# Kernel tuning notes

Measured on AMD Instinct MI355X. Metric: run time of the kernel, lower is better.

The kernel has to match this reference:

```python
import jax, jax.numpy as jnp
import numpy as np

S, N, F, E, H = 64, 1000, 64, 128, 2  # seq_len, nodes/graph, node_dim, emb_dim, heads
DEG = 8
C = E // H  # per-head channels


def setup_inputs() -> dict:
    key = jax.random.key(0)
    ks = jax.random.split(key, 16)
    Ntot = S * N
    Eg = N * DEG
    src = jax.random.randint(ks[0], (S, Eg), 0, N)
    dst = jax.random.randint(ks[1], (S, Eg), 0, N)
    off = (jnp.arange(S) * N)[:, None]
    edge_index = jnp.stack([(src + off).reshape(-1), (dst + off).reshape(-1)]).astype(jnp.int32)
    nfm = jax.random.normal(ks[2], (Ntot, F), jnp.float32)
    reachable = jax.random.uniform(ks[3], (S, N)) > 0.2
    reachable = reachable.at[:, 0].set(True)  # ensure each row has a reachable node
    h0 = jnp.zeros((N, E), jnp.float32)
    c0 = jnp.zeros((N, E), jnp.float32)

    def lin(k, i, o):
        return (jax.random.normal(k, (i, o), jnp.float32) / np.sqrt(i)).astype(jnp.float32)

    return dict(
        nfm=nfm, edge_index=edge_index, reachable=reachable, h0=h0, c0=c0,
        gat_W1=lin(ks[4], F, E), gat_b1=jnp.zeros((E,), jnp.float32),
        gat_att1=(jax.random.normal(ks[5], (H, C), jnp.float32) / np.sqrt(C)).astype(jnp.float32),
        gat_bias1=jnp.zeros((E,), jnp.float32),
        gat_W=(jax.random.normal(ks[6], (4, E, E), jnp.float32) / np.sqrt(E)).astype(jnp.float32),
        gat_b=jnp.zeros((4, E), jnp.float32),
        gat_att=(jax.random.normal(ks[7], (4, H, C), jnp.float32) / np.sqrt(C)).astype(jnp.float32),
        gat_bias=jnp.zeros((4, E), jnp.float32),
        lstm_Wih=(jax.random.normal(ks[8], (4 * E, E), jnp.float32) / np.sqrt(E)).astype(jnp.float32),
        lstm_Whh=(jax.random.normal(ks[9], (4 * E, E), jnp.float32) / np.sqrt(E)).astype(jnp.float32),
        lstm_bih=jnp.zeros((4 * E,), jnp.float32), lstm_bhh=jnp.zeros((4 * E,), jnp.float32),
        th6_W=lin(ks[10], E, E), th6_b=jnp.zeros((E,), jnp.float32),
        th7_W=lin(ks[11], E, E), th7_b=jnp.zeros((E,), jnp.float32),
        th5_W=lin(ks[12], 2 * E, 1), th5_b=jnp.zeros((1,), jnp.float32),
    )


def _gat_layer(x, src, dst, W, b, att, bias, Ntot):
    # GATv2Conv, share_weights=True: x_l == x_r = lin(x)
    Hh, Ch = att.shape
    xl = (x @ W + b).reshape(-1, Hh, Ch)                 # [Ntot,H,C]
    e = jax.nn.leaky_relu(xl[src] + xl[dst], 0.2)        # [Etot,H,C]
    logit = jnp.einsum('ehc,hc->eh', e, att)             # [Etot,H]
    m = jax.ops.segment_max(logit, dst, num_segments=Ntot)
    a = jnp.exp(logit - m[dst])                          # segment-stable softmax
    denom = jax.ops.segment_sum(a, dst, num_segments=Ntot)
    alpha = a / denom[dst]
    out = jax.ops.segment_sum(xl[src] * alpha[:, :, None], dst, num_segments=Ntot)
    return out.reshape(-1, Hh * Ch) + bias               # concat heads + bias


def _forward(nfm, edge_index, reachable, h0, c0, gat_W1, gat_b1, gat_att1, gat_bias1,
             gat_W, gat_b, gat_att, gat_bias, lstm_Wih, lstm_Whh, lstm_bih, lstm_bhh,
             th6_W, th6_b, th7_W, th7_b, th5_W, th5_b):
    Ntot = nfm.shape[0]
    loops = jnp.arange(Ntot, dtype=edge_index.dtype)     # add_self_loops=True
    src = jnp.concatenate([edge_index[0], loops])
    dst = jnp.concatenate([edge_index[1], loops])

    x = jax.nn.relu(_gat_layer(nfm, src, dst, gat_W1, gat_b1, gat_att1, gat_bias1, Ntot))
    for i in range(4):  # layers 2..5; no activation after last
        x = _gat_layer(x, src, dst, gat_W[i], gat_b[i], gat_att[i], gat_bias[i], Ntot)
        if i < 3:
            x = jax.nn.relu(x)

    mu = x.reshape(S, N, E)                              # [seq, batch(=nodes), emb]

    def step(carry, xt):
        h, c = carry
        g = xt @ lstm_Wih.T + lstm_bih + h @ lstm_Whh.T + lstm_bhh
        i_, f_, gg, o_ = jnp.split(g, 4, axis=-1)        # torch gate order i,f,g,o
        c = jax.nn.sigmoid(f_) * c + jax.nn.sigmoid(i_) * jnp.tanh(gg)
        h = jax.nn.sigmoid(o_) * jnp.tanh(c)
        return (h, c), h

    (hT, cT), mu = jax.lax.scan(step, (h0, c0), mu)      # mu: [S,N,E]

    meanpool = mu.mean(axis=1, keepdims=True)            # [S,1,E]
    gs = meanpool @ th6_W + th6_b
    la = mu @ th7_W + th7_b
    rep = jax.nn.relu(jnp.concatenate([jnp.broadcast_to(gs, la.shape), la], axis=-1))
    logits = (rep @ th5_W)[..., 0] + th5_b               # [S,N]
    logits = jnp.where(reachable, logits, -jnp.inf)
    prob = jax.nn.softmax(logits, axis=1)
    return prob, hT, cT


def reference(nfm, edge_index, reachable, h0, c0, gat_W1, gat_b1, gat_att1, gat_bias1,
              gat_W, gat_b, gat_att, gat_bias, lstm_Wih, lstm_Whh, lstm_bih, lstm_bhh,
              th6_W, th6_b, th7_W, th7_b, th5_W, th5_b):
    return _forward(nfm, edge_index, reachable, h0, c0, gat_W1, gat_b1, gat_att1, gat_bias1,
                    gat_W, gat_b, gat_att, gat_bias, lstm_Wih, lstm_Whh, lstm_bih, lstm_bhh,
                    th6_W, th6_b, th7_W, th7_b, th5_W, th5_b)
```

## Files before the change

kernel.cpp:

```cpp
#include <hip/hip_runtime.h>
#include <hip/hip_bf16.h>

#define SQ   64
#define NN   1000
#define NT   64000
#define EE   128
#define EG   512000
#define ET   576000

#define WS_XA      0ull
#define WS_XB      33000000ull
#define WS_ROWPTR  66000000ull
#define WS_CURSOR  66300000ull
#define WS_SRCS    66600000ull
#define WS_INCL    69000000ull
#define WS_BSUM    69300000ull
#define WS_BOFF    69302048ull
#define WS_MODE    69304096ull
#define WS_WQA     70000000ull
#define WS_WQB     70262144ull
#define WS_AS      70600000ull
#define WS_LOGIT2  70700000ull
#define WS2_XC     33000000ull
#define WS2_BFRAG  164100000ull
#define WS2_GHI    164300000ull
#define WS2_GLO    164650000ull
#define WS2_B512   165000000ull
#define WS2_MODE   165010000ull
#define WS2_AS     165020000ull
#define WS2_LOGIT2 165100000ull
#define WS2_NEED   165360000ull
#define G_W1    0
#define G_WL    8192
#define G_PROJ  73728
#define G_W7    139264

typedef __attribute__((ext_vector_type(8))) short short8;
typedef __attribute__((ext_vector_type(4))) float f32x4;

__device__ __forceinline__ float rdlane(float v, int l) {
    return __int_as_float(__builtin_amdgcn_readlane(__float_as_int(v), l));
}
__device__ __forceinline__ float sigm(float x) { return 1.0f / (1.0f + __expf(-x)); }
__device__ __forceinline__ float tanh_f(float x) {
    x = fminf(fmaxf(x, -30.0f), 30.0f);
    float e = __expf(2.0f * x);
    return (e - 1.0f) / (e + 1.0f);
}
__device__ __forceinline__ float tanh2(float x) {
    return 2.0f / (1.0f + __expf(-2.0f * x)) - 1.0f;
}
__device__ __forceinline__ ushort f2bf(float x) {
    unsigned u = __float_as_uint(x);
    unsigned r = (u + 0x7FFFu + ((u >> 16) & 1u)) >> 16;
    return (ushort)r;
}
__device__ __forceinline__ float bf2f(ushort h) {
    return __uint_as_float(((unsigned)h) << 16);
}

__global__ void detect_mode_k(const unsigned char* __restrict__ p, int* __restrict__ mode) {
    __shared__ int f0, f3;
    const int t = threadIdx.x;
    if (t == 0) { f0 = 0; f3 = 0; }
    __syncthreads();
    int l0 = 0, l3 = 0;
    for (int i = t; i < 16000; i += 256) {
        if (p[4 * i])     l0 = 1;
        if (p[4 * i + 3]) l3 = 1;
    }
    if (l0) atomicOr(&f0, 1);
    if (l3) atomicOr(&f3, 1);
    __syncthreads();
    if (t == 0) {
        int m;
        if (f0 && f3)      m = 1;
        else if (f0)       m = 0;
        else               m = 2;
        *mode = m;
    }
}

__global__ void zero_ints_k(int* __restrict__ p, int n) {
    int i = blockIdx.x * 256 + threadIdx.x;
    if (i < n) p[i] = 0;
}
__global__ void hist_k(const int* __restrict__ ei, int* __restrict__ deg) {
    int e = blockIdx.x * 256 + threadIdx.x;
    if (e < ET) {
        int d = (e < EG) ? ei[EG + e] : (e - EG);
        atomicAdd(deg + d, 1);
    }
}
__global__ void scan1_k(const int* __restrict__ deg, int* __restrict__ incl, int* __restrict__ bsum) {
    __shared__ int sh[256];
    const int t = threadIdx.x;
    const int i = blockIdx.x * 256 + t;
    sh[t] = deg[i];
    __syncthreads();
    for (int o = 1; o < 256; o <<= 1) {
        int add = (t >= o) ? sh[t - o] : 0;
        __syncthreads();
        sh[t] += add;
        __syncthreads();
    }
    incl[i] = sh[t];
    if (t == 255) bsum[blockIdx.x] = sh[255];
}
__global__ void scan2_k(const int* __restrict__ bsum, int* __restrict__ boff) {
    __shared__ int sh[256];
    const int t = threadIdx.x;
    int v = (t < 250) ? bsum[t] : 0;
    sh[t] = v;
    __syncthreads();
    for (int o = 1; o < 256; o <<= 1) {
        int add = (t >= o) ? sh[t - o] : 0;
        __syncthreads();
        sh[t] += add;
        __syncthreads();
    }
    if (t < 250) boff[t] = sh[t] - v;
}
__global__ void scan3_k(const int* __restrict__ incl, const int* __restrict__ boff,
                        int* __restrict__ rowptr, int* __restrict__ cursor_deg) {
    const int i = blockIdx.x * 256 + threadIdx.x;
    int total = incl[i] + boff[blockIdx.x];
    int excl  = total - cursor_deg[i];
    rowptr[i] = excl;
    cursor_deg[i] = excl;
    if (i == NT - 1) rowptr[NT] = total;
}
__global__ void fill_k(const int* __restrict__ ei, int* __restrict__ cursor, int* __restrict__ srcs) {
    int e = blockIdx.x * 256 + threadIdx.x;
    if (e < ET) {
        int s_, d_;
        if (e < EG) { s_ = ei[e]; d_ = ei[EG + e]; }
        else        { s_ = e - EG; d_ = s_; }
        int p = atomicAdd(cursor + d_, 1);
        srcs[p] = s_;
    }
}

__device__ __forceinline__ void gfrag_dev(const float* __restrict__ src, const int ks,
                                          const int ns, const int K,
                                          ushort* __restrict__ dhi, ushort* __restrict__ dlo,
                                          const int total, const int id) {
    if (id < total) {
        int j = id & 7, lane = (id >> 3) & 63;
        int f = id >> 9;
        int KT = K >> 5;
        int nt = f / KT, kt = f - nt * KT;
        int n = nt * 16 + (lane & 15);
        int k = kt * 32 + ((lane >> 4) << 3) + j;
        float v = src[(size_t)k * ks + (size_t)n * ns];
        ushort h = f2bf(v);
        dhi[id] = h;
        dlo[id] = f2bf(v - bf2f(h));
    }
}
__global__ void build_all_k(const float* __restrict__ Whh, const float* __restrict__ bih,
                            const float* __restrict__ bhh, const float* __restrict__ W1,
                            const float* __restrict__ Wl, const float* __restrict__ Wih,
                            const float* __restrict__ W7, ushort* __restrict__ Bfrag,
                            float* __restrict__ b512, ushort* __restrict__ ghi,
                            ushort* __restrict__ glo) {
    const int b = blockIdx.x, t = threadIdx.x;
    if (b < 256) {
        int id = b * 256 + t;
        int j = id & 7, lane = (id >> 3) & 63, kt = (id >> 9) & 3, tile = id >> 11;
        int gate = tile * 16 + (lane & 15);
        int k = kt * 32 + ((lane >> 4) << 3) + j;
        Bfrag[id] = f2bf(Whh[(size_t)gate * 128 + k]);
    } else if (b < 258) {
        int i = (b - 256) * 256 + t;
        if (i < 512) b512[i] = bih[i] + bhh[i];
    } else if (b < 290) {
        gfrag_dev(W1, 128, 1, 64, ghi + G_W1, glo + G_W1, 8192, (b - 258) * 256 + t);
    } else if (b < 546) {
        int bb = b - 290;
        int i = bb >> 6;
        gfrag_dev(Wl + (size_t)i * 16384, 128, 1, 128,
                  ghi + G_WL + i * 16384, glo + G_WL + i * 16384, 16384, (bb & 63) * 256 + t);
    } else if (b < 802) {
        gfrag_dev(Wih, 1, 128, 128, ghi + G_PROJ, glo + G_PROJ, 65536, (b - 546) * 256 + t);
    } else {
        gfrag_dev(W7, 128, 1, 128, ghi + G_W7, glo + G_W7, 16384, (b - 802) * 256 + t);
    }
}

template <int KT>
__global__ __launch_bounds__(256) void gemm_mf(
    const float* __restrict__ x, const ushort* __restrict__ bhi,
    const ushort* __restrict__ blo, const float* __restrict__ bias,
    float* __restrict__ out, const int ldout)
{
    constexpr int K = KT * 32;
    __shared__ __align__(16) ushort ahi_s[KT * 4 * 64 * 8];
    __shared__ __align__(16) ushort alo_s[KT * 4 * 64 * 8];
    const int t = threadIdx.x;
    const int w = t >> 6, lane = t & 63;
    const int quad = lane >> 4, col = lane & 15;
    const int row0 = blockIdx.x * 64;
    const int col0 = blockIdx.y * 128;

    {
        const int r  = t >> 2;
        const int kc = (t & 3) * (K / 4);
        const int rw = r >> 4, rcol = r & 15;
        const float* xr = x + (size_t)(row0 + r) * K + kc;
#pragma unroll
        for (int k = 0; k < K / 4; k += 4) {
            const int ch = kc + k;
            const int idx = (((ch >> 5) * 4 + rw) * 64 + ((ch >> 3) & 3) * 16 + rcol) * 8
                            + (ch & 7);
            float4 v = *(const float4*)(xr + k);
            ushort h0_ = f2bf(v.x), h1_ = f2bf(v.y), h2_ = f2bf(v.z), h3_ = f2bf(v.w);
            ushort l0_ = f2bf(v.x - bf2f(h0_)), l1_ = f2bf(v.y - bf2f(h1_));
            ushort l2_ = f2bf(v.z - bf2f(h2_)), l3_ = f2bf(v.w - bf2f(h3_));
            *(uint2*)(ahi_s + idx) = make_uint2((uint)h0_ | ((uint)h1_ << 16),
                                                (uint)h2_ | ((uint)h3_ << 16));
            *(uint2*)(alo_s + idx) = make_uint2((uint)l0_ | ((uint)l1_ << 16),
                                                (uint)l2_ | ((uint)l3_ << 16));
        }
    }
    __syncthreads();

    short8 ah[KT], al[KT];
#pragma unroll
    for (int kt = 0; kt < KT; kt++) {
        const int off = ((kt * 4 + w) * 64 + lane) * 8;
        ah[kt] = *(const short8*)(ahi_s + off);
        al[kt] = *(const short8*)(alo_s + off);
    }

    f32x4 acc[8];
#pragma unroll
    for (int q = 0; q < 8; q++) acc[q] = (f32x4){0.f, 0.f, 0.f, 0.f};

#pragma unroll
    for (int q = 0; q < 8; q++) {
#pragma unroll
        for (int kt = 0; kt < KT; kt++) {
            const int f = ((((col0 >> 4) + q) * KT + kt) * 64 + lane) * 8;
            short8 bh = *(const short8*)(bhi + f);
            short8 bl = *(const short8*)(blo + f);
            acc[q] = __builtin_amdgcn_mfma_f32_16x16x32_bf16(ah[kt], bh, acc[q], 0, 0, 0);
            acc[q] = __builtin_amdgcn_mfma_f32_16x16x32_bf16(al[kt], bh, acc[q], 0, 0, 0);
            acc[q] = __builtin_amdgcn_mfma_f32_16x16x32_bf16(ah[kt], bl, acc[q], 0, 0, 0);
        }
    }

#pragma unroll
    for (int q = 0; q < 8; q++) {
        float bv = bias[col0 + q * 16 + col];
#pragma unroll
        for (int r = 0; r < 4; r++) {
            out[(size_t)(row0 + w * 16 + quad * 4 + r) * ldout + col0 + q * 16 + col]
                = acc[q][r] + bv;
        }
    }
}

template <int K>
__global__ __launch_bounds__(256) void gemm3(
    const float* __restrict__ x, const float* __restrict__ W,
    const float* __restrict__ b, float* __restrict__ out)
{
    __shared__ float Wsh[64 * 128];
    __shared__ float xT[64][132];
    const int t = threadIdx.x;
    const int row0 = blockIdx.x * 128;
    const int cg = t & 15;
    const int rg = t >> 4;
    float4 acc[8][2];
#pragma unroll
    for (int r = 0; r < 8; r++) {
        acc[r][0] = make_float4(0.f, 0.f, 0.f, 0.f);
        acc[r][1] = make_float4(0.f, 0.f, 0.f, 0.f);
    }
    for (int k0 = 0; k0 < K; k0 += 64) {
        for (int i = t * 4; i < 64 * 128; i += 1024)
            *(float4*)(Wsh + i) = *(const float4*)(W + (size_t)k0 * 128 + i);
        for (int i = t * 4; i < 128 * 64; i += 1024) {
            int r = i >> 6, k = i & 63;
            float4 v = *(const float4*)(x + (size_t)(row0 + r) * K + k0 + k);
            xT[k + 0][r] = v.x; xT[k + 1][r] = v.y;
            xT[k + 2][r] = v.z; xT[k + 3][r] = v.w;
        }
        __syncthreads();
#pragma unroll 2
        for (int k = 0; k < 64; k++) {
            float4 w0 = *(const float4*)(Wsh + k * 128 + cg * 8);
            float4 w1 = *(const float4*)(Wsh + k * 128 + cg * 8 + 4);
            float4 x0 = *(const float4*)(&xT[k][rg * 8]);
            float4 x1 = *(const float4*)(&xT[k][rg * 8 + 4]);
            float xv[8] = {x0.x, x0.y, x0.z, x0.w, x1.x, x1.y, x1.z, x1.w};
#pragma unroll
            for (int r = 0; r < 8; r++) {
                acc[r][0].x += xv[r] * w0.x; acc[r][0].y += xv[r] * w0.y;
                acc[r][0].z += xv[r] * w0.z; acc[r][0].w += xv[r] * w0.w;
                acc[r][1].x += xv[r] * w1.x; acc[r][1].y += xv[r] * w1.y;
                acc[r][1].z += xv[r] * w1.z; acc[r][1].w += xv[r] * w1.w;
            }
        }
        __syncthreads();
    }
    float4 bv0 = *(const float4*)(b + cg * 8);
    float4 bv1 = *(const float4*)(b + cg * 8 + 4);
#pragma unroll
    for (int r = 0; r < 8; r++) {
        float4 o0, o1;
        o0.x = acc[r][0].x + bv0.x; o0.y = acc[r][0].y + bv0.y;
        o0.z = acc[r][0].z + bv0.z; o0.w = acc[r][0].w + bv0.w;
        o1.x = acc[r][1].x + bv1.x; o1.y = acc[r][1].y + bv1.y;
        o1.z = acc[r][1].z + bv1.z; o1.w = acc[r][1].w + bv1.w;
        float* op = out + (size_t)(row0 + rg * 8 + r) * 128 + cg * 8;
        *(float4*)(op) = o0;
        *(float4*)(op + 4) = o1;
    }
}

__global__ __launch_bounds__(256) void gat_fused_k(
    const float* __restrict__ xl, const int* __restrict__ rowptr,
    const int* __restrict__ srcs, const float* __restrict__ att,
    const float* __restrict__ bias, float* __restrict__ out, const int do_relu)
{
    const int lane = threadIdx.x & 63;
    const int q = lane & 31;
    const int h = lane >> 5;
    const int b = blockIdx.x;
    const int g = b & 7;
    const int j = b >> 3;
    const int jq = j / 250;
    const int jj = j - jq * 250;
    const int s = g + 8 * jq;
    const int n = s * NN + jj * 4 + (threadIdx.x >> 6);

    const float4 a4 = *(const float4*)(att + q * 4);
    const float4 xd = *(const float4*)(xl + (size_t)n * 128 + q * 4);
    const int i0 = rowptr[n], i1 = rowptr[n + 1];

    float mA = -1e30f, dA = 0.f, axA = 0.f, ayA = 0.f, azA = 0.f, awA = 0.f;
    float mB = -1e30f, dB = 0.f, axB = 0.f, ayB = 0.f, azB = 0.f, awB = 0.f;

    int iA = i0 + h, iB = i0 + h + 2;
    int svA = (iA < i1) ? srcs[iA] : 0;
    int svB = (iB < i1) ? srcs[iB] : 0;
    float4 xsA = *(const float4*)(xl + (size_t)svA * 128 + q * 4);
    float4 xsB = *(const float4*)(xl + (size_t)svB * 128 + q * 4);

    for (int base = i0; base < i1; base += 4) {
        const bool vA = (iA < i1), vB = (iB < i1);
        const int svA2 = (iA + 4 < i1) ? srcs[iA + 4] : 0;
        const int svB2 = (iB + 4 < i1) ? srcs[iB + 4] : 0;
        const float4 xA2 = *(const float4*)(xl + (size_t)svA2 * 128 + q * 4);
        const float4 xB2 = *(const float4*)(xl + (size_t)svB2 * 128 + q * 4);

        float uA0 = xsA.x + xd.x, uA1 = xsA.y + xd.y;
        float uA2 = xsA.z + xd.z, uA3 = xsA.w + xd.w;
        float uB0 = xsB.x + xd.x, uB1 = xsB.y + xd.y;
        float uB2 = xsB.z + xd.z, uB3 = xsB.w + xd.w;
        float pA, pB;
        pA  = a4.x * fmaxf(uA0, 0.2f * uA0);
        pA += a4.y * fmaxf(uA1, 0.2f * uA1);
        pA += a4.z * fmaxf(uA2, 0.2f * uA2);
        pA += a4.w * fmaxf(uA3, 0.2f * uA3);
        pB  = a4.x * fmaxf(uB0, 0.2f * uB0);
        pB += a4.y * fmaxf(uB1, 0.2f * uB1);
        pB += a4.z * fmaxf(uB2, 0.2f * uB2);
        pB += a4.w * fmaxf(uB3, 0.2f * uB3);
        pA += __shfl_xor(pA, 1);   pB += __shfl_xor(pB, 1);
        pA += __shfl_xor(pA, 2);   pB += __shfl_xor(pB, 2);
        pA += __shfl_xor(pA, 4);   pB += __shfl_xor(pB, 4);
        pA += __shfl_xor(pA, 8);   pB += __shfl_xor(pB, 8);

        float mnA = fmaxf(mA, vA ? pA : -1e30f);
        float mnB = fmaxf(mB, vB ? pB : -1e30f);
        float scA = __expf(mA - mnA), scB = __expf(mB - mnB);
        float wA = vA ? __expf(pA - mnA) : 0.f;
        float wB = vB ? __expf(pB - mnB) : 0.f;
        dA  = dA  * scA + wA;          dB  = dB  * scB + wB;
        axA = axA * scA + wA * xsA.x;  axB = axB * scB + wB * xsB.x;
        ayA = ayA * scA + wA * xsA.y;  ayB = ayB * scB + wB * xsB.y;
        azA = azA * scA + wA * xsA.z;  azB = azB * scB + wB * xsB.z;
        awA = awA * scA + wA * xsA.w;  awB = awB * scB + wB * xsB.w;
        mA = mnA; mB = mnB;
        xsA = xA2; xsB = xB2;
        iA += 4; iB += 4;
    }

    float m1 = fmaxf(mA, mB);
    float sA = __expf(mA - m1), sB = __expf(mB - m1);
    float d  = dA * sA + dB * sB;
    float ax = axA * sA + axB * sB;
    float ay = ayA * sA + ayB * sB;
    float az = azA * sA + azB * sB;
    float aw = awA * sA + awB * sB;
    float m  = m1;

    float m2 = __shfl_xor(m, 32);
    float d2 = __shfl_xor(d, 32);
    float bx = __shfl_xor(ax, 32);
    float by = __shfl_xor(ay, 32);
    float bz = __shfl_xor(az, 32);
    float bw = __shfl_xor(aw, 32);
    float mm = fmaxf(m, m2);
    float s1 = __expf(m - mm), s2 = __expf(m2 - mm);
    float den = d * s1 + d2 * s2;
    float inv = 1.f / den;
    float4 bv = *(const float4*)(bias + q * 4);
    float ox = (ax * s1 + bx * s2) * inv + bv.x;
    float oy = (ay * s1 + by * s2) * inv + bv.y;
    float oz = (az * s1 + bz * s2) * inv + bv.z;
    float ow = (aw * s1 + bw * s2) * inv + bv.w;
    if (do_relu) {
        ox = fmaxf(ox, 0.f); oy = fmaxf(oy, 0.f);
        oz = fmaxf(oz, 0.f); ow = fmaxf(ow, 0.f);
    }
    if (lane < 32)
        *(float4*)(out + (size_t)n * 128 + q * 4) = make_float4(ox, oy, oz, ow);
}

__global__ void build_wq_k(const float* __restrict__ Wih, const float* __restrict__ Whh,
                           float4* __restrict__ WQa, float4* __restrict__ WQb) {
    int id = blockIdx.x * 256 + threadIdx.x;
    if (id < 64 * 256) {
        int kp = id >> 8, t = id & 255;
        int j1 = t, j2 = t + 256;
        WQa[id] = make_float4(Wih[(size_t)j1 * 128 + 2 * kp], Whh[(size_t)j1 * 128 + 2 * kp],
                              Wih[(size_t)j1 * 128 + 2 * kp + 1], Whh[(size_t)j1 * 128 + 2 * kp + 1]);
        WQb[id] = make_float4(Wih[(size_t)j2 * 128 + 2 * kp], Whh[(size_t)j2 * 128 + 2 * kp],
                              Wih[(size_t)j2 * 128 + 2 * kp + 1], Whh[(size_t)j2 * 128 + 2 * kp + 1]);
    }
}

#define LSTM_GROUP(buf, gbase)                                                     \
    _Pragma("unroll")                                                              \
    for (int i_ = 0; i_ < 4; i_++) {                                               \
        const int kp_ = (gbase) * 4 + i_;                                          \
        const float4 qa_ = buf[i_];                                                \
        const float4 qb_ = buf[4 + i_];                                            \
        _Pragma("unroll")                                                          \
        for (int n_ = 0; n_ < 4; n_++) {                                           \
            const float sx0_ = rdlane(xr[n_].x, kp_);                              \
            const float sh0_ = rdlane(hr[n_].x, kp_);                              \
            const float sx1_ = rdlane(xr[n_].y, kp_);                              \
            const float sh1_ = rdlane(hr[n_].y, kp_);                              \
            acc1[n_] += sx0_ * qa_.x + sh0_ * qa_.y + sx1_ * qa_.z + sh1_ * qa_.w; \
            acc2[n_] += sx0_ * qb_.x + sh0_ * qb_.y + sx1_ * qb_.z + sh1_ * qb_.w; \
        }                                                                          \
    }

__global__ __launch_bounds__(256, 1) void lstm_k(
    float* __restrict__ mu, const float4* __restrict__ WQa, const float4* __restrict__ WQb,
    const float* __restrict__ bih, const float* __restrict__ bhh,
    const float* __restrict__ h0, const float* __restrict__ c0,
    float* __restrict__ hT, float* __restrict__ cT)
{
    const int t = threadIdx.x, lane = t & 63;
    const int n0 = blockIdx.x * 4;
    __shared__ float hsh[4][128];
    __shared__ float gsh[4][512];
    const float b1 = bih[t] + bhh[t];
    const float b2 = bih[t + 256] + bhh[t + 256];
    float creg[2];
#pragma unroll
    for (int q = 0; q < 2; q++) {
        int id = t + 256 * q;
        creg[q] = c0[(size_t)(n0 + (id >> 7)) * 128 + (id & 127)];
    }
    for (int i = t; i < 512; i += 256)
        hsh[i >> 7][i & 127] = h0[(size_t)(n0 + (i >> 7)) * 128 + (i & 127)];

    const float4* pA = WQa + t;
    const float4* pB = WQb + t;

    float2 xr[4], xnx[4];
#pragma unroll
    for (int n = 0; n < 4; n++)
        xr[n] = *(const float2*)(mu + (size_t)n0 * 128 + n * 128 + lane * 2);
    __syncthreads();

    for (int s = 0; s < SQ; s++) {
        float* xrow = mu + ((size_t)s * NN + n0) * 128;
        float2 hr[4];
#pragma unroll
        for (int n = 0; n < 4; n++) hr[n] = *(const float2*)(&hsh[n][lane * 2]);

        float4 bufA[8], bufB[8];
#pragma unroll
        for (int i = 0; i < 4; i++) { bufA[i] = pA[i * 256]; bufA[4 + i] = pB[i * 256]; }

        if (s + 1 < SQ) {
            const float* xrow2 = mu + ((size_t)(s + 1) * NN + n0) * 128;
#pragma unroll
            for (int n = 0; n < 4; n++) xnx[n] = *(const float2*)(xrow2 + n * 128 + lane * 2);
        }

        float acc1[4], acc2[4];
#pragma unroll
        for (int n = 0; n < 4; n++) { acc1[n] = b1; acc2[n] = b2; }

        for (int g = 0; g < 16; g += 2) {
#pragma unroll
            for (int i = 0; i < 4; i++) {
                bufB[i]     = pA[((g + 1) * 4 + i) * 256];
                bufB[4 + i] = pB[((g + 1) * 4 + i) * 256];
            }
            LSTM_GROUP(bufA, g)
            if (g < 14) {
#pragma unroll
                for (int i = 0; i < 4; i++) {
                    bufA[i]     = pA[((g + 2) * 4 + i) * 256];
                    bufA[4 + i] = pB[((g + 2) * 4 + i) * 256];
                }
            }
            LSTM_GROUP(bufB, g + 1)
        }

#pragma unroll
        for (int n = 0; n < 4; n++) { gsh[n][t] = acc1[n]; gsh[n][t + 256] = acc2[n]; }
        __syncthreads();
#pragma unroll
        for (int q = 0; q < 2; q++) {
            int id = t + 256 * q;
            int n = id >> 7, e = id & 127;
            float iv = gsh[n][e], fv = gsh[n][128 + e];
            float gv = gsh[n][256 + e], ov = gsh[n][384 + e];
            float c = sigm(fv) * creg[q] + sigm(iv) * tanh_f(gv);
            float h = sigm(ov) * tanh_f(c);
            creg[q] = c;
            hsh[n][e] = h;
            xrow[n * 128 + e] = h;
            if (s == SQ - 1) {
                hT[(size_t)(n0 + n) * 128 + e] = h;
                cT[(size_t)(n0 + n) * 128 + e] = c;
            }
        }
#pragma unroll
        for (int n = 0; n < 4; n++) xr[n] = xnx[n];
        __syncthreads();
    }
}

__global__ __launch_bounds__(512, 2) void lstm8_k(
    float* __restrict__ mu, const float* __restrict__ xC,
    const ushort* __restrict__ Bfrag,
    const float* __restrict__ h0, const float* __restrict__ c0,
    float* __restrict__ hT, float* __restrict__ cT)
{
    const int t = threadIdx.x;
    const int w = t >> 6, lane = t & 63;
    const int quad = lane >> 4, col = lane & 15;
    const int n0 = blockIdx.x * 4;
    const int enode = t >> 7;
    const int ech   = t & 127;

    __shared__ __align__(16) ushort hbuf[2][2][16 * 136];
    __shared__ float gsh[4][512];

    short8 bf[4][4];
#pragma unroll
    for (int g4 = 0; g4 < 4; g4++)
#pragma unroll
        for (int kt = 0; kt < 4; kt++) {
            int tile = g4 * 8 + w;
            bf[g4][kt] = *(const short8*)(Bfrag + (((tile * 4 + kt) * 64 + lane) << 3));
        }

    for (int i = t; i < 2048; i += 512) {
        int node = i >> 7, ee = i & 127;
        float v = (node < 4) ? h0[(size_t)(n0 + node) * 128 + ee] : 0.f;
        ushort hh = f2bf(v), hl = f2bf(v - bf2f(hh));
        hbuf[0][0][node * 136 + ee] = hh; hbuf[0][1][node * 136 + ee] = hl;
        hbuf[1][0][node * 136 + ee] = hh; hbuf[1][1][node * 136 + ee] = hl;
    }
    float cst = c0[(size_t)(n0 + enode) * 128 + ech];

    float xcr[4], xcn[4];
#pragma unroll
    for (int g4 = 0; g4 < 4; g4++)
        xcr[g4] = xC[((size_t)(n0 + enode)) * 512 + g4 * 128 + ech];
    __syncthreads();

    int p = 0;
    for (int s = 0; s < SQ; s++) {
        if (s + 1 < SQ) {
            const float* xn = xC + ((size_t)(s + 1) * NN + n0 + enode) * 512;
#pragma unroll
            for (int g4 = 0; g4 < 4; g4++)
                xcn[g4] = xn[g4 * 128 + ech];
        }

        short8 ahi[4], alo[4];
#pragma unroll
        for (int kt = 0; kt < 4; kt++) {
            ahi[kt] = *(const short8*)(&hbuf[p][0][col * 136 + kt * 32 + quad * 8]);
            alo[kt] = *(const short8*)(&hbuf[p][1][col * 136 + kt * 32 + quad * 8]);
        }

        f32x4 acc[4];
#pragma unroll
        for (int g4 = 0; g4 < 4; g4++) acc[g4] = (f32x4){0.f, 0.f, 0.f, 0.f};
#pragma unroll
        for (int kt = 0; kt < 4; kt++) {
#pragma unroll
            for (int g4 = 0; g4 < 4; g4++)
                acc[g4] = __builtin_amdgcn_mfma_f32_16x16x32_bf16(ahi[kt], bf[g4][kt], acc[g4], 0, 0, 0);
#pragma unroll
            for (int g4 = 0; g4 < 4; g4++)
                acc[g4] = __builtin_amdgcn_mfma_f32_16x16x32_bf16(alo[kt], bf[g4][kt], acc[g4], 0, 0, 0);
        }

        if (quad == 0) {
#pragma unroll
            for (int g4 = 0; g4 < 4; g4++)
#pragma unroll
                for (int r = 0; r < 4; r++)
                    gsh[r][(g4 * 8 + w) * 16 + col] = acc[g4][r];
        }
        __syncthreads();

        {
            float iv = gsh[enode][0 * 128 + ech] + xcr[0];
            float fv = gsh[enode][1 * 128 + ech] + xcr[1];
            float gv = gsh[enode][2 * 128 + ech] + xcr[2];
            float ov = gsh[enode][3 * 128 + ech] + xcr[3];
            float c = sigm(fv) * cst + sigm(iv) * tanh2(gv);
            float h = sigm(ov) * tanh2(c);
            cst = c;
            const int pn = p ^ 1;
            ushort hh = f2bf(h);
            hbuf[pn][0][enode * 136 + ech] = hh;
            hbuf[pn][1][enode * 136 + ech] = f2bf(h - bf2f(hh));
            mu[((size_t)s * NN + n0 + enode) * 128 + ech] = h;
            if (s == SQ - 1) {
                hT[(size_t)(n0 + enode) * 128 + ech] = h;
                cT[(size_t)(n0 + enode) * 128 + ech] = c;
            }
            p = pn;
        }
#pragma unroll
        for (int g4 = 0; g4 < 4; g4++) xcr[g4] = xcn[g4];
        __syncthreads();
    }
}

__global__ __launch_bounds__(256) void meanpool_gs_k(
    const float* __restrict__ mu, const float* __restrict__ W6,
    const float* __restrict__ b6, const float* __restrict__ w5,
    float* __restrict__ A)
{
    const int s = blockIdx.x, t = threadIdx.x;
    const int ch = t & 127, half = t >> 7;
    __shared__ float mp[128];
    __shared__ float red[256];
    float acc = 0.f;
    for (int n = half * 500; n < (half + 1) * 500; n++)
        acc += mu[((size_t)s * NN + n) * 128 + ch];
    red[t] = acc;
    __syncthreads();
    if (t < 128) mp[t] = (red[t] + red[t + 128]) * 0.001f;
    __syncthreads();
    float g = 0.f;
    if (t < 128) {
        g = b6[t];
        for (int k = 0; k < 128; k++) g += mp[k] * W6[(size_t)k * 128 + t];
        g = fmaxf(g, 0.f) * w5[t];
    }
    red[t] = g;
    __syncthreads();
    for (int o = 128; o > 0; o >>= 1) {
        if (t < o) red[t] += red[t + o];
        __syncthreads();
    }
    if (t == 0) A[s] = red[0];
}

__global__ __launch_bounds__(256) void rowdot_k(
    const float* __restrict__ la, const float* __restrict__ w5,
    const float* __restrict__ b5, const float* __restrict__ A,
    float* __restrict__ out)
{
    const int lane = threadIdx.x & 63;
    const int row = blockIdx.x * 4 + (threadIdx.x >> 6);
    float2 v = *(const float2*)(la + (size_t)row * 128 + lane * 2);
    float2 w = *(const float2*)(w5 + 128 + lane * 2);
    float x = fmaxf(v.x, 0.f) * w.x + fmaxf(v.y, 0.f) * w.y;
#pragma unroll
    for (int o = 32; o; o >>= 1) x += __shfl_down(x, o);
    if (lane == 0) out[row] = x + A[row / NN] + b5[0];
}

__device__ __forceinline__ bool reach_at(const void* reach, int mode, int idx) {
    if (mode == 0) return ((const int*)reach)[idx] != 0;
    if (mode == 1) return ((const unsigned char*)reach)[idx] != 0;
    return ((const float*)reach)[idx] != 0.f;
}
__global__ __launch_bounds__(256) void softmax_k(
    const float* __restrict__ lg, const void* __restrict__ reach,
    const int* __restrict__ mode, float* __restrict__ prob)
{
    const int s = blockIdx.x, t = threadIdx.x;
    const int m = *mode;
    __shared__ float red[256];
    float mx = -1e30f;
    for (int i = t; i < NN; i += 256) {
        int idx = s * NN + i;
        if (reach_at(reach, m, idx)) mx = fmaxf(mx, lg[idx]);
    }
    red[t] = mx;
    __syncthreads();
    for (int o = 128; o; o >>= 1) {
        if (t < o) red[t] = fmaxf(red[t], red[t + o]);
        __syncthreads();
    }
    mx = red[0];
    __syncthreads();
    float sum = 0.f;
    for (int i = t; i < NN; i += 256) {
        int idx = s * NN + i;
        float v = reach_at(reach, m, idx) ? __expf(lg[idx] - mx) : 0.f;
        prob[idx] = v;
        sum += v;
    }
    red[t] = sum;
    __syncthreads();
    for (int o = 128; o; o >>= 1) {
        if (t < o) red[t] += red[t + o];
        __syncthreads();
    }
    float inv = 1.f / red[0];
    for (int i = t; i < NN; i += 256) prob[s * NN + i] *= inv;
}

extern "C" void kernel_launch(void* const* d_in, const int* in_sizes, int n_in,
                              void* d_out, int out_size, void* d_ws, size_t ws_size,
                              hipStream_t stream) {
    const float* nfm   = (const float*)d_in[0];
    const int*   ei    = (const int*)d_in[1];
    const void*  reach = d_in[2];
    const float* h0    = (const float*)d_in[3];
    const float* c0    = (const float*)d_in[4];
    const float* W1    = (const float*)d_in[5];
    const float* b1    = (const float*)d_in[6];
    const float* att1  = (const float*)d_in[7];
    const float* bias1 = (const float*)d_in[8];
    const float* Wl    = (const float*)d_in[9];
    const float* bl    = (const float*)d_in[10];
    const float* attl  = (const float*)d_in[11];
    const float* biasl = (const float*)d_in[12];
    const float* Wih   = (const float*)d_in[13];
    const float* Whh   = (const float*)d_in[14];
    const float* bih   = (const float*)d_in[15];
    const float* bhh   = (const float*)d_in[16];
    const float* W6    = (const float*)d_in[17];
    const float* b6    = (const float*)d_in[18];
    const float* W7    = (const float*)d_in[19];
    const float* b7    = (const float*)d_in[20];
    const float* w5    = (const float*)d_in[21];
    const float* b5    = (const float*)d_in[22];

    char* ws = (char*)d_ws;
    const bool bigws = (ws_size >= WS2_NEED);

    float*  xA     = (float*)(ws + WS_XA);
    float*  xB     = (float*)(ws + WS_XB);
    int*    rowptr = (int*)(ws + WS_ROWPTR);
    int*    cursor = (int*)(ws + WS_CURSOR);
    int*    srcs   = (int*)(ws + WS_SRCS);
    int*    incl   = (int*)(ws + WS_INCL);
    int*    bsum   = (int*)(ws + WS_BSUM);
    int*    boff   = (int*)(ws + WS_BOFF);
    int*    modep  = bigws ? (int*)(ws + WS2_MODE)     : (int*)(ws + WS_MODE);
    float*  As     = bigws ? (float*)(ws + WS2_AS)     : (float*)(ws + WS_AS);
    float*  logit2 = bigws ? (float*)(ws + WS2_LOGIT2) : (float*)(ws + WS_LOGIT2);
    float*  xC     = (float*)(ws + WS2_XC);
    ushort* Bfrag  = (ushort*)(ws + WS2_BFRAG);
    ushort* ghi    = (ushort*)(ws + WS2_GHI);
    ushort* glo    = (ushort*)(ws + WS2_GLO);
    float*  b512   = (float*)(ws + WS2_B512);
    float4* WQa    = (float4*)(ws + WS_WQA);
    float4* WQb    = (float4*)(ws + WS_WQB);

    float* prob = (float*)d_out;
    float* hT   = (float*)d_out + 64000;
    float* cT   = (float*)d_out + 192000;

    detect_mode_k<<<1, 256, 0, stream>>>((const unsigned char*)reach, modep);
    zero_ints_k<<<250, 256, 0, stream>>>(cursor, NT);
    hist_k<<<2250, 256, 0, stream>>>(ei, cursor);
    scan1_k<<<250, 256, 0, stream>>>(cursor, incl, bsum);
    scan2_k<<<1, 256, 0, stream>>>(bsum, boff);
    scan3_k<<<250, 256, 0, stream>>>(incl, boff, rowptr, cursor);
    fill_k<<<2250, 256, 0, stream>>>(ei, cursor, srcs);
    if (bigws) {
        build_all_k<<<866, 256, 0, stream>>>(Whh, bih, bhh, W1, Wl, Wih, W7,
                                             Bfrag, b512, ghi, glo);
    } else {
        build_wq_k<<<64, 256, 0, stream>>>(Wih, Whh, WQa, WQb);
    }

    for (int l = 0; l < 5; l++) {
        if (bigws) {
            if (l == 0)
                gemm_mf<2><<<dim3(1000, 1), 256, 0, stream>>>(nfm, ghi + G_W1, glo + G_W1, b1, xB, 128);
            else
                gemm_mf<4><<<dim3(1000, 1), 256, 0, stream>>>(xA, ghi + G_WL + (l - 1) * 16384,
                                                              glo + G_WL + (l - 1) * 16384,
                                                              bl + (l - 1) * 128, xB, 128);
        } else {
            if (l == 0)
                gemm3<64><<<500, 256, 0, stream>>>(nfm, W1, b1, xB);
            else
                gemm3<128><<<500, 256, 0, stream>>>(xA, Wl + (size_t)(l - 1) * 128 * 128,
                                                    bl + (l - 1) * 128, xB);
        }
        const float* att  = (l == 0) ? att1  : attl  + (l - 1) * 128;
        const float* bias = (l == 0) ? bias1 : biasl + (l - 1) * 128;
        gat_fused_k<<<16000, 256, 0, stream>>>(xB, rowptr, srcs, att, bias, xA,
                                               (l < 4) ? 1 : 0);
    }

    if (bigws) {
        gemm_mf<4><<<dim3(1000, 4), 256, 0, stream>>>(xA, ghi + G_PROJ, glo + G_PROJ, b512, xC, 512);
        lstm8_k<<<250, 512, 0, stream>>>(xA, xC, Bfrag, h0, c0, hT, cT);
    } else {
        lstm_k<<<250, 256, 0, stream>>>(xA, WQa, WQb, bih, bhh, h0, c0, hT, cT);
    }

    meanpool_gs_k<<<64, 256, 0, stream>>>(xA, W6, b6, w5, As);
    if (bigws)
        gemm_mf<4><<<dim3(1000, 1), 256, 0, stream>>>(xA, ghi + G_W7, glo + G_W7, b7, xB, 128);
    else
        gemm3<128><<<500, 256, 0, stream>>>(xA, W7, b7, xB);
    rowdot_k<<<16000, 256, 0, stream>>>(xB, w5, b5, As, logit2);
    softmax_k<<<64, 256, 0, stream>>>(logit2, reach, modep, prob);
}
```

Baseline: 667.3 us.

## Fuse W7 GEMM with head dot, drop row-constant meanpool term

Adds gemm_w7dot, which computes the th7 projection with split-bf16 MFMA and immediately applies relu, multiplies by the second half of th5 and reduces each row to a logit. This removes the la intermediate write/read and the separate rowdot launch. The meanpool/global-state term and b5 are dropped because they add a per-sequence constant that cancels in the softmax, which removes the meanpool kernel. The detect_mode kernel is also widened to 1024 threads.

```diff
diff --git a/kernel.cpp b/kernel.cpp
--- a/kernel.cpp
+++ b/kernel.cpp
@@ -19,7 +19,6 @@
 #define WS_MODE    69304096ull
 #define WS_WQA     70000000ull
 #define WS_WQB     70262144ull
-#define WS_AS      70600000ull
 #define WS_LOGIT2  70700000ull
 #define WS2_XC     33000000ull
 #define WS2_BFRAG  164100000ull
@@ -27,7 +26,6 @@
 #define WS2_GLO    164650000ull
 #define WS2_B512   165000000ull
 #define WS2_MODE   165010000ull
-#define WS2_AS     165020000ull
 #define WS2_LOGIT2 165100000ull
 #define WS2_NEED   165360000ull
 #define G_W1    0
@@ -65,7 +63,7 @@
     if (t == 0) { f0 = 0; f3 = 0; }
     __syncthreads();
     int l0 = 0, l3 = 0;
-    for (int i = t; i < 16000; i += 256) {
+    for (int i = t; i < 16000; i += 1024) {
         if (p[4 * i])     l0 = 1;
         if (p[4 * i + 3]) l3 = 1;
     }
@@ -261,6 +259,93 @@
     }
 }
 
+__global__ __launch_bounds__(256) void gemm_w7dot(
+    const float* __restrict__ x, const ushort* __restrict__ bhi,
+    const ushort* __restrict__ blo, const float* __restrict__ bias,
+    const float* __restrict__ w5h, float* __restrict__ logit2)
+{
+    constexpr int KT = 4;
+    constexpr int K = 128;
+    __shared__ __align__(16) ushort ahi_s[KT * 4 * 64 * 8];
+    __shared__ __align__(16) ushort alo_s[KT * 4 * 64 * 8];
+    const int t = threadIdx.x;
+    const int w = t >> 6, lane = t & 63;
+    const int quad = lane >> 4, col = lane & 15;
+    const int row0 = blockIdx.x * 64;
+
+    {
+        const int r  = t >> 2;
+        const int kc = (t & 3) * (K / 4);
+        const int rw = r >> 4, rcol = r & 15;
+        const float* xr = x + (size_t)(row0 + r) * K + kc;
+#pragma unroll
+        for (int k = 0; k < K / 4; k += 4) {
+            const int ch = kc + k;
+            const int idx = (((ch >> 5) * 4 + rw) * 64 + ((ch >> 3) & 3) * 16 + rcol) * 8
+                            + (ch & 7);
+            float4 v = *(const float4*)(xr + k);
+            ushort h0_ = f2bf(v.x), h1_ = f2bf(v.y), h2_ = f2bf(v.z), h3_ = f2bf(v.w);
+            ushort l0_ = f2bf(v.x - bf2f(h0_)), l1_ = f2bf(v.y - bf2f(h1_));
+            ushort l2_ = f2bf(v.z - bf2f(h2_)), l3_ = f2bf(v.w - bf2f(h3_));
+            *(uint2*)(ahi_s + idx) = make_uint2((uint)h0_ | ((uint)h1_ << 16),
+                                                (uint)h2_ | ((uint)h3_ << 16));
+            *(uint2*)(alo_s + idx) = make_uint2((uint)l0_ | ((uint)l1_ << 16),
+                                                (uint)l2_ | ((uint)l3_ << 16));
+        }
+    }
+    __syncthreads();
+
+    short8 ah[KT], al[KT];
+#pragma unroll
+    for (int kt = 0; kt < KT; kt++) {
+        const int off = ((kt * 4 + w) * 64 + lane) * 8;
+        ah[kt] = *(const short8*)(ahi_s + off);
+        al[kt] = *(const short8*)(alo_s + off);
+    }
+
+    f32x4 acc[8];
+#pragma unroll
+    for (int q = 0; q < 8; q++) acc[q] = (f32x4){0.f, 0.f, 0.f, 0.f};
+
+#pragma unroll
+    for (int q = 0; q < 8; q++) {
+#pragma unroll
+        for (int kt = 0; kt < KT; kt++) {
+            const int f = ((q * KT + kt) * 64 + lane) * 8;
+            short8 bh = *(const short8*)(bhi + f);
+            short8 bl = *(const short8*)(blo + f);
+            acc[q] = __builtin_amdgcn_mfma_f32_16x16x32_bf16(ah[kt], bh, acc[q], 0, 0, 0);
+            acc[q] = __builtin_amdgcn_mfma_f32_16x16x32_bf16(al[kt], bh, acc[q], 0, 0, 0);
+            acc[q] = __builtin_amdgcn_mfma_f32_16x16x32_bf16(ah[kt], bl, acc[q], 0, 0, 0);
+        }
+    }
+
+    float part0 = 0.f, part1 = 0.f, part2 = 0.f, part3 = 0.f;
+#pragma unroll
+    for (int q = 0; q < 8; q++) {
+        float bv = bias[q * 16 + col];
+        float wv = w5h[q * 16 + col];
+        part0 += fmaxf(acc[q][0] + bv, 0.f) * wv;
+        part1 += fmaxf(acc[q][1] + bv, 0.f) * wv;
+        part2 += fmaxf(acc[q][2] + bv, 0.f) * wv;
+        part3 += fmaxf(acc[q][3] + bv, 0.f) * wv;
+    }
+#pragma unroll
+    for (int o = 1; o < 16; o <<= 1) {
+        part0 += __shfl_xor(part0, o);
+        part1 += __shfl_xor(part1, o);
+        part2 += __shfl_xor(part2, o);
+        part3 += __shfl_xor(part3, o);
+    }
+    if (col == 0) {
+        const int rbase = row0 + w * 16 + quad * 4;
+        logit2[rbase + 0] = part0;
+        logit2[rbase + 1] = part1;
+        logit2[rbase + 2] = part2;
+        logit2[rbase + 3] = part3;
+    }
+}
+
 template <int K>
 __global__ __launch_bounds__(256) void gemm3(
     const float* __restrict__ x, const float* __restrict__ W,
@@ -646,40 +731,8 @@
     }
 }
 
-__global__ __launch_bounds__(256) void meanpool_gs_k(
-    const float* __restrict__ mu, const float* __restrict__ W6,
-    const float* __restrict__ b6, const float* __restrict__ w5,
-    float* __restrict__ A)
-{
-    const int s = blockIdx.x, t = threadIdx.x;
-    const int ch = t & 127, half = t >> 7;
-    __shared__ float mp[128];
-    __shared__ float red[256];
-    float acc = 0.f;
-    for (int n = half * 500; n < (half + 1) * 500; n++)
-        acc += mu[((size_t)s * NN + n) * 128 + ch];
-    red[t] = acc;
-    __syncthreads();
-    if (t < 128) mp[t] = (red[t] + red[t + 128]) * 0.001f;
-    __syncthreads();
-    float g = 0.f;
-    if (t < 128) {
-        g = b6[t];
-        for (int k = 0; k < 128; k++) g += mp[k] * W6[(size_t)k * 128 + t];
-        g = fmaxf(g, 0.f) * w5[t];
-    }
-    red[t] = g;
-    __syncthreads();
-    for (int o = 128; o > 0; o >>= 1) {
-        if (t < o) red[t] += red[t + o];
-        __syncthreads();
-    }
-    if (t == 0) A[s] = red[0];
-}
-
 __global__ __launch_bounds__(256) void rowdot_k(
     const float* __restrict__ la, const float* __restrict__ w5,
-    const float* __restrict__ b5, const float* __restrict__ A,
     float* __restrict__ out)
 {
     const int lane = threadIdx.x & 63;
@@ -689,7 +742,7 @@
     float x = fmaxf(v.x, 0.f) * w.x + fmaxf(v.y, 0.f) * w.y;
 #pragma unroll
     for (int o = 32; o; o >>= 1) x += __shfl_down(x, o);
-    if (lane == 0) out[row] = x + A[row / NN] + b5[0];
+    if (lane == 0) out[row] = x;
 }
 
 __device__ __forceinline__ bool reach_at(const void* reach, int mode, int idx) {
@@ -760,6 +813,7 @@
     const float* b7    = (const float*)d_in[20];
     const float* w5    = (const float*)d_in[21];
     const float* b5    = (const float*)d_in[22];
+    (void)W6; (void)b6; (void)b5;
 
     char* ws = (char*)d_ws;
     const bool bigws = (ws_size >= WS2_NEED);
@@ -773,7 +827,6 @@
     int*    bsum   = (int*)(ws + WS_BSUM);
     int*    boff   = (int*)(ws + WS_BOFF);
     int*    modep  = bigws ? (int*)(ws + WS2_MODE)     : (int*)(ws + WS_MODE);
-    float*  As     = bigws ? (float*)(ws + WS2_AS)     : (float*)(ws + WS_AS);
     float*  logit2 = bigws ? (float*)(ws + WS2_LOGIT2) : (float*)(ws + WS_LOGIT2);
     float*  xC     = (float*)(ws + WS2_XC);
     ushort* Bfrag  = (ushort*)(ws + WS2_BFRAG);
@@ -787,7 +840,7 @@
     float* hT   = (float*)d_out + 64000;
     float* cT   = (float*)d_out + 192000;
 
-    detect_mode_k<<<1, 256, 0, stream>>>((const unsigned char*)reach, modep);
+    detect_mode_k<<<1, 1024, 0, stream>>>((const unsigned char*)reach, modep);
     zero_ints_k<<<250, 256, 0, stream>>>(cursor, NT);
     hist_k<<<2250, 256, 0, stream>>>(ei, cursor);
     scan1_k<<<250, 256, 0, stream>>>(cursor, incl, bsum);
@@ -829,11 +882,11 @@
         lstm_k<<<250, 256, 0, stream>>>(xA, WQa, WQb, bih, bhh, h0, c0, hT, cT);
     }
 
-    meanpool_gs_k<<<64, 256, 0, stream>>>(xA, W6, b6, w5, As);
-    if (bigws)
-        gemm_mf<4><<<dim3(1000, 1), 256, 0, stream>>>(xA, ghi + G_W7, glo + G_W7, b7, xB, 128);
-    else
+    if (bigws) {
+        gemm_w7dot<<<1000, 256, 0, stream>>>(xA, ghi + G_W7, glo + G_W7, b7, w5 + 128, logit2);
+    } else {
         gemm3<128><<<500, 256, 0, stream>>>(xA, W7, b7, xB);
-    rowdot_k<<<16000, 256, 0, stream>>>(xB, w5, b5, As, logit2);
+        rowdot_k<<<16000, 256, 0, stream>>>(xB, w5, logit2);
+    }
     softmax_k<<<64, 256, 0, stream>>>(logit2, reach, modep, prob);
 }
```

Result: faster. 626.5 us (-6.1%).
